# Optimization experiments

Hardware: AMD Instinct MI355X
Metric: run time of the kernel (lower is better)

Reference implementation:

```python
import jax, jax.numpy as jnp
import numpy as np

NUM_TOKENS = 16384
DIM = 4096
N_EXPERTS = 256
ROUTE_SCALE = 1.0


def setup_inputs() -> dict:
    key = jax.random.key(0)
    k_x, k_w = jax.random.split(key)
    x = jax.random.normal(k_x, (NUM_TOKENS, DIM), dtype=jnp.float32)
    # nn.init.normal_(weight, std=0.02)
    weight = 0.02 * jax.random.normal(k_w, (N_EXPERTS, DIM), dtype=jnp.float32)
    return {"x": x, "weight": weight}


def reference(x, weight):
    # Router GEMM: [T, D] @ [D, E] -> [T, E]
    scores = jnp.einsum("td,ed->te", x, weight)
    # Eval-mode token_choice path: softmax in fp32
    probs = jax.nn.softmax(scores.astype(jnp.float32), axis=-1)  # [T, E]
    indices = jnp.argmax(probs, axis=-1, keepdims=True)  # [T, 1] int
    # Hard one-hot scatter of argmax
    y_hard = jax.nn.one_hot(indices[:, 0], N_EXPERTS, dtype=probs.dtype)  # [T, E]
    # Straight-through estimator mix
    ste = jax.lax.stop_gradient(y_hard - probs) + probs
    # Gather routing weight at the selected expert
    weights = jnp.take_along_axis(ste, indices, axis=-1)  # [T, 1]
    weights = (weights * ROUTE_SCALE).astype(x.dtype)
    return weights, indices
```

## Files before the change

kernel.cpp:

```cpp
#include <hip/hip_runtime.h>
#include <hip/hip_bf16.h>
#include <stdint.h>

#define NUM_TOKENS 16384
#define DIM        4096
#define NEXP       256
#define MB         32
#define NKB        (DIM / 32)
#define NWAVES     4
#define MARGIN     0.025f
#define CAP        16384

typedef __attribute__((ext_vector_type(4))) float   f32x4;
typedef __attribute__((ext_vector_type(8))) __bf16  bf16x8;

static __device__ __forceinline__ bf16x8 pack8(float4 u, float4 v) {
    union { bf16x8 v8; __hip_bfloat162 h[4]; } r;
    r.h[0] = __float22bfloat162_rn(float2{u.x, u.y});
    r.h[1] = __float22bfloat162_rn(float2{u.z, u.w});
    r.h[2] = __float22bfloat162_rn(float2{v.x, v.y});
    r.h[3] = __float22bfloat162_rn(float2{v.z, v.w});
    return r.v8;
}

__global__ void pack_weights(const float* __restrict__ w,
                             __hip_bfloat16* __restrict__ P,
                             int* __restrict__ counter) {
    if (blockIdx.x == 0 && threadIdx.x == 0) *counter = 0;
    const int gid  = blockIdx.x * blockDim.x + threadIdx.x;
    const int kb   = gid >> 10;
    const int rem  = gid & 1023;
    const int g    = rem >> 6;
    const int lane = rem & 63;
    const int e    = g * 16 + (lane & 15);
    const int k    = kb * 32 + (lane >> 4) * 8;
    const float4 u = *(const float4*)(w + (size_t)e * DIM + k);
    const float4 v = *(const float4*)(w + (size_t)e * DIM + k + 4);
    *(bf16x8*)(P + (size_t)gid * 8) = pack8(u, v);
}

__global__ __launch_bounds__(256, 4) void gate_main(
    const float* __restrict__ x,
    const __hip_bfloat16* __restrict__ P,
    float* __restrict__ out,
    int* __restrict__ counter,
    int4* __restrict__ entries)
{
    __shared__ float4 cand[NWAVES][MB];

    const int tid  = threadIdx.x;
    const int wv   = tid >> 6;
    const int lane = tid & 63;
    const int quad = lane >> 4;
    const int col  = lane & 15;
    const int tok0 = blockIdx.x * MB;

    const float* xr0 = x + (size_t)(tok0 + col) * DIM + quad * 8;
    const float* xr1 = x + (size_t)(tok0 + 16 + col) * DIM + quad * 8;
    const __hip_bfloat16* Pw = P + (size_t)(wv * 4) * 512 + (size_t)lane * 8;

    f32x4 acc[2][4];
    #pragma unroll
    for (int mt = 0; mt < 2; ++mt)
        #pragma unroll
        for (int nt = 0; nt < 4; ++nt)
            acc[mt][nt] = f32x4{0.f, 0.f, 0.f, 0.f};

    for (int kb = 0; kb < NKB; ++kb) {
        const int koff = kb * 32;
        float4 a00 = *(const float4*)(xr0 + koff);
        float4 a01 = *(const float4*)(xr0 + koff + 4);
        float4 a10 = *(const float4*)(xr1 + koff);
        float4 a11 = *(const float4*)(xr1 + koff + 4);
        bf16x8 bh[4];
        #pragma unroll
        for (int nt = 0; nt < 4; ++nt)
            bh[nt] = *(const bf16x8*)(Pw + (size_t)kb * 8192 + nt * 512);
        bf16x8 ah0 = pack8(a00, a01);
        bf16x8 ah1 = pack8(a10, a11);
        #pragma unroll
        for (int nt = 0; nt < 4; ++nt) {
            acc[0][nt] = __builtin_amdgcn_mfma_f32_16x16x32_bf16(ah0, bh[nt], acc[0][nt], 0, 0, 0);
            acc[1][nt] = __builtin_amdgcn_mfma_f32_16x16x32_bf16(ah1, bh[nt], acc[1][nt], 0, 0, 0);
        }
    }

    #pragma unroll
    for (int mt = 0; mt < 2; ++mt) {
        #pragma unroll
        for (int r = 0; r < 4; ++r) {
            float t1s = acc[mt][0][r]; int t1e = wv * 64 + col;
            float t2s = acc[mt][1][r]; int t2e = t1e + 16;
            if (t2s > t1s) { float ts = t1s; int te = t1e; t1s = t2s; t1e = t2e; t2s = ts; t2e = te; }
            #pragma unroll
            for (int nt = 2; nt < 4; ++nt) {
                float s = acc[mt][nt][r]; int e = wv * 64 + nt * 16 + col;
                if (s > t1s)      { t2s = t1s; t2e = t1e; t1s = s; t1e = e; }
                else if (s > t2s) { t2s = s; t2e = e; }
            }
            #pragma unroll
            for (int m = 1; m <= 8; m <<= 1) {
                float o1s = __shfl_xor(t1s, m); int o1e = __shfl_xor(t1e, m);
                float o2s = __shfl_xor(t2s, m); int o2e = __shfl_xor(t2e, m);
                bool o1_top = (o1s > t1s) || (o1s == t1s && o1e < t1e);
                if (o1_top) {
                    bool keep_t1 = (t1s > o2s) || (t1s == o2s && t1e < o2e);
                    t2s = keep_t1 ? t1s : o2s; t2e = keep_t1 ? t1e : o2e;
                    t1s = o1s; t1e = o1e;
                } else {
                    bool o1_2nd = (o1s > t2s) || (o1s == t2s && o1e < t2e);
                    if (o1_2nd) { t2s = o1s; t2e = o1e; }
                }
            }
            if (col == 0) {
                int tok = mt * 16 + quad * 4 + r;
                cand[wv][tok] = make_float4(t1s, __int_as_float(t1e), t2s, __int_as_float(t2e));
            }
        }
    }
    __syncthreads();

    if (tid < MB) {
        float4 c0 = cand[0][tid];
        float t1s = c0.x; int t1e = __float_as_int(c0.y);
        float t2s = c0.z; int t2e = __float_as_int(c0.w);
        #pragma unroll
        for (int wvi = 1; wvi < NWAVES; ++wvi) {
            float4 c = cand[wvi][tid];
            float o1s = c.x; int o1e = __float_as_int(c.y);
            float o2s = c.z; int o2e = __float_as_int(c.w);
            bool o1_top = (o1s > t1s) || (o1s == t1s && o1e < t1e);
            if (o1_top) {
                bool keep_t1 = (t1s > o2s) || (t1s == o2s && t1e < o2e);
                t2s = keep_t1 ? t1s : o2s; t2e = keep_t1 ? t1e : o2e;
                t1s = o1s; t1e = o1e;
            } else {
                bool o1_2nd = (o1s > t2s) || (o1s == t2s && o1e < t2e);
                if (o1_2nd) { t2s = o1s; t2e = o1e; }
            }
        }
        const int gtok = tok0 + tid;
        out[gtok] = 1.0f;
        out[NUM_TOKENS + gtok] = (float)t1e;
        if (t1s - t2s < MARGIN) {
            int slot = atomicAdd(counter, 1);
            if (slot < CAP) entries[slot] = make_int4(gtok, t1e, t2e, 0);
        }
    }
}

__global__ void refine(const float* __restrict__ x,
                       const float* __restrict__ w,
                       const int* __restrict__ counter,
                       const int4* __restrict__ entries,
                       float* __restrict__ out) {
    const int gwave  = (blockIdx.x * blockDim.x + threadIdx.x) >> 6;
    const int lane   = threadIdx.x & 63;
    const int nwaves = (gridDim.x * blockDim.x) >> 6;
    int n = *counter; if (n > CAP) n = CAP;
    for (int i = gwave; i < n; i += nwaves) {
        int4 e = entries[i];
        const float* xr = x + (size_t)e.x * DIM;
        const float* w1 = w + (size_t)e.y * DIM;
        const float* w2 = w + (size_t)e.z * DIM;
        double d1 = 0.0, d2 = 0.0;
        for (int k = lane; k < DIM; k += 64) {
            double xv = (double)xr[k];
            d1 += xv * (double)w1[k];
            d2 += xv * (double)w2[k];
        }
        #pragma unroll
        for (int m = 32; m > 0; m >>= 1) {
            d1 += __shfl_xor(d1, m);
            d2 += __shfl_xor(d2, m);
        }
        if (lane == 0) {
            int best = (d1 > d2) ? e.y : ((d2 > d1) ? e.z : (e.y < e.z ? e.y : e.z));
            out[NUM_TOKENS + e.x] = (float)best;
        }
    }
}

extern "C" void kernel_launch(void* const* d_in, const int* in_sizes, int n_in,
                              void* d_out, int out_size, void* d_ws, size_t ws_size,
                              hipStream_t stream) {
    const float* x = (const float*)d_in[0];
    const float* w = (const float*)d_in[1];
    float* out = (float*)d_out;

    char* ws = (char*)d_ws;
    __hip_bfloat16* P = (__hip_bfloat16*)ws;
    int*  counter = (int*)(ws + (2u << 20));
    int4* entries = (int4*)(ws + (2u << 20) + 16);

    pack_weights<<<NKB * 16 * 64 / 256, 256, 0, stream>>>(w, P, counter);
    gate_main<<<NUM_TOKENS / MB, 256, 0, stream>>>(x, P, out, counter, entries);
    refine<<<256, 256, 0, stream>>>(x, w, counter, entries, out);
}
```

Measured before the change: 536.6 us.

## Stage bf16-converted token tile in LDS and widen block to 64 tokens

The gate GEMM now processes 64 tokens per block with 8 waves, each wave owning 32 experts. Coalesced fp32 x rows are loaded once, converted to bf16 and staged in padded shared memory, and each wave reads its A fragments from LDS. The next phase's x loads are issued early to overlap with the MFMAs. The aim is better coalescing of x and fewer redundant x conversions per expert group, at the cost of more LDS traffic, two barriers per phase and higher register pressure.

```diff
diff --git a/kernel.cpp b/kernel.cpp
--- a/kernel.cpp
+++ b/kernel.cpp
@@ -5,9 +5,12 @@
 #define NUM_TOKENS 16384
 #define DIM        4096
 #define NEXP       256
-#define MB         32
+#define MB         64
+#define BKP        256
+#define NPH        (DIM / BKP)
 #define NKB        (DIM / 32)
-#define NWAVES     4
+#define APAD       264
+#define NWAVES     8
 #define MARGIN     0.025f
 #define CAP        16384
 
@@ -21,6 +24,12 @@
     r.h[2] = __float22bfloat162_rn(float2{v.x, v.y});
     r.h[3] = __float22bfloat162_rn(float2{v.z, v.w});
     return r.v8;
+}
+static __device__ __forceinline__ ushort4 cvt4(float4 u) {
+    union { ushort4 u4; __hip_bfloat162 h[2]; } r;
+    r.h[0] = __float22bfloat162_rn(float2{u.x, u.y});
+    r.h[1] = __float22bfloat162_rn(float2{u.z, u.w});
+    return r.u4;
 }
 
 __global__ void pack_weights(const float* __restrict__ w,
@@ -39,13 +48,14 @@
     *(bf16x8*)(P + (size_t)gid * 8) = pack8(u, v);
 }
 
-__global__ __launch_bounds__(256, 4) void gate_main(
+__global__ __launch_bounds__(512, 2) void gate_main(
     const float* __restrict__ x,
     const __hip_bfloat16* __restrict__ P,
     float* __restrict__ out,
     int* __restrict__ counter,
     int4* __restrict__ entries)
 {
+    __shared__ unsigned short lAh[MB][APAD];
     __shared__ float4 cand[NWAVES][MB];
 
     const int tid  = threadIdx.x;
@@ -55,49 +65,67 @@
     const int col  = lane & 15;
     const int tok0 = blockIdx.x * MB;
 
-    const float* xr0 = x + (size_t)(tok0 + col) * DIM + quad * 8;
-    const float* xr1 = x + (size_t)(tok0 + 16 + col) * DIM + quad * 8;
-    const __hip_bfloat16* Pw = P + (size_t)(wv * 4) * 512 + (size_t)lane * 8;
-
-    f32x4 acc[2][4];
+    const int xcol = (lane) * 4;
+    const float* xbase = x + (size_t)tok0 * DIM;
+
+    const __hip_bfloat16* Pw = P + ((size_t)(wv * 2) * 64 + lane) * 8;
+
+    f32x4 acc[4][2];
     #pragma unroll
-    for (int mt = 0; mt < 2; ++mt)
-        #pragma unroll
-        for (int nt = 0; nt < 4; ++nt)
+    for (int mt = 0; mt < 4; ++mt)
+        #pragma unroll
+        for (int nt = 0; nt < 2; ++nt)
             acc[mt][nt] = f32x4{0.f, 0.f, 0.f, 0.f};
 
-    for (int kb = 0; kb < NKB; ++kb) {
-        const int koff = kb * 32;
-        float4 a00 = *(const float4*)(xr0 + koff);
-        float4 a01 = *(const float4*)(xr0 + koff + 4);
-        float4 a10 = *(const float4*)(xr1 + koff);
-        float4 a11 = *(const float4*)(xr1 + koff + 4);
-        bf16x8 bh[4];
-        #pragma unroll
-        for (int nt = 0; nt < 4; ++nt)
-            bh[nt] = *(const bf16x8*)(Pw + (size_t)kb * 8192 + nt * 512);
-        bf16x8 ah0 = pack8(a00, a01);
-        bf16x8 ah1 = pack8(a10, a11);
-        #pragma unroll
-        for (int nt = 0; nt < 4; ++nt) {
-            acc[0][nt] = __builtin_amdgcn_mfma_f32_16x16x32_bf16(ah0, bh[nt], acc[0][nt], 0, 0, 0);
-            acc[1][nt] = __builtin_amdgcn_mfma_f32_16x16x32_bf16(ah1, bh[nt], acc[1][nt], 0, 0, 0);
-        }
-    }
-
+    float4 xv[8];
     #pragma unroll
-    for (int mt = 0; mt < 2; ++mt) {
+    for (int r = 0; r < 8; ++r)
+        xv[r] = *(const float4*)(xbase + (size_t)(r * 8 + wv) * DIM + xcol);
+
+    for (int p = 0; p < NPH; ++p) {
+        const int k0 = p * BKP;
+
+        __syncthreads();
+        #pragma unroll
+        for (int r = 0; r < 8; ++r)
+            *(ushort4*)&lAh[r * 8 + wv][xcol] = cvt4(xv[r]);
+        __syncthreads();
+
+        bf16x8 bh[8][2];
+        #pragma unroll
+        for (int kk = 0; kk < 8; ++kk) {
+            const size_t kb16 = (size_t)(p * 8 + kk) * 16;
+            bh[kk][0] = *(const bf16x8*)(Pw + (kb16 + 0) * 512);
+            bh[kk][1] = *(const bf16x8*)(Pw + (kb16 + 1) * 512);
+        }
+        if (p + 1 < NPH) {
+            #pragma unroll
+            for (int r = 0; r < 8; ++r)
+                xv[r] = *(const float4*)(xbase + (size_t)(r * 8 + wv) * DIM + k0 + BKP + xcol);
+        }
+        #pragma unroll
+        for (int kk = 0; kk < 8; ++kk) {
+            bf16x8 ah[4];
+            #pragma unroll
+            for (int mt = 0; mt < 4; ++mt)
+                ah[mt] = *(const bf16x8*)&lAh[mt * 16 + col][kk * 32 + quad * 8];
+            #pragma unroll
+            for (int mt = 0; mt < 4; ++mt) {
+                acc[mt][0] = __builtin_amdgcn_mfma_f32_16x16x32_bf16(ah[mt], bh[kk][0], acc[mt][0], 0, 0, 0);
+                acc[mt][1] = __builtin_amdgcn_mfma_f32_16x16x32_bf16(ah[mt], bh[kk][1], acc[mt][1], 0, 0, 0);
+            }
+        }
+    }
+
+    #pragma unroll
+    for (int mt = 0; mt < 4; ++mt) {
         #pragma unroll
         for (int r = 0; r < 4; ++r) {
-            float t1s = acc[mt][0][r]; int t1e = wv * 64 + col;
-            float t2s = acc[mt][1][r]; int t2e = t1e + 16;
-            if (t2s > t1s) { float ts = t1s; int te = t1e; t1s = t2s; t1e = t2e; t2s = ts; t2e = te; }
-            #pragma unroll
-            for (int nt = 2; nt < 4; ++nt) {
-                float s = acc[mt][nt][r]; int e = wv * 64 + nt * 16 + col;
-                if (s > t1s)      { t2s = t1s; t2e = t1e; t1s = s; t1e = e; }
-                else if (s > t2s) { t2s = s; t2e = e; }
-            }
+            float s0 = acc[mt][0][r]; int e0 = wv * 32 + col;
+            float s1 = acc[mt][1][r]; int e1 = e0 + 16;
+            float t1s, t2s; int t1e, t2e;
+            if (s1 > s0) { t1s = s1; t1e = e1; t2s = s0; t2e = e0; }
+            else         { t1s = s0; t1e = e0; t2s = s1; t2e = e1; }
             #pragma unroll
             for (int m = 1; m <= 8; m <<= 1) {
                 float o1s = __shfl_xor(t1s, m); int o1e = __shfl_xor(t1e, m);
@@ -194,6 +222,6 @@
     int4* entries = (int4*)(ws + (2u << 20) + 16);
 
     pack_weights<<<NKB * 16 * 64 / 256, 256, 0, stream>>>(w, P, counter);
-    gate_main<<<NUM_TOKENS / MB, 256, 0, stream>>>(x, P, out, counter, entries);
+    gate_main<<<NUM_TOKENS / MB, 512, 0, stream>>>(x, P, out, counter, entries);
     refine<<<256, 256, 0, stream>>>(x, w, counter, entries, out);
 }
```

After: 455.9 us. -15.0%, faster.
